# Kernel tuning notes

Measured on AMD Instinct MI355X. Metric: run time of the kernel, lower is better.

Reference implementation:

```python
import jax, jax.numpy as jnp
import numpy as np

N_PROBLEMS = 20000
N_SKILLS = 1000
EMB_SIZE = 128
TIME_LOG = 5.0
B, L = 64, 1024


def setup_inputs() -> dict:
    key = jax.random.key(0)
    ks = jax.random.split(key, 10)
    skills = jax.random.randint(ks[0], (B, L), 0, N_SKILLS)
    problems = jax.random.randint(ks[1], (B, L), 0, N_PROBLEMS)
    labels = jax.random.randint(ks[2], (B, L), 0, 2)
    times = jnp.sort(jax.random.randint(ks[3], (B, L), 0, 1_000_000), axis=-1)
    inp = jnp.stack([skills, problems, labels, times], axis=1)  # [B,4,L]
    std = 0.01
    return {
        "input": inp,
        "problem_base": std * jax.random.normal(ks[4], (N_PROBLEMS, 1), jnp.float32),
        "skill_base": std * jax.random.normal(ks[5], (N_SKILLS, 1), jnp.float32),
        "alpha_inter": std * jax.random.normal(ks[6], (N_SKILLS * 2, EMB_SIZE), jnp.float32),
        "alpha_skill": std * jax.random.normal(ks[7], (N_SKILLS, EMB_SIZE), jnp.float32),
        "beta_inter": std * jax.random.normal(ks[8], (N_SKILLS * 2, EMB_SIZE), jnp.float32),
        "beta_skill": std * jax.random.normal(ks[9], (N_SKILLS, EMB_SIZE), jnp.float32),
    }


def reference(input, problem_base, skill_base, alpha_inter, alpha_skill, beta_inter, beta_skill):
    skills = input[:, 0]    # [B,L]
    problems = input[:, 1]
    labels = input[:, 2]
    times = input[:, 3]

    mask_labels = labels * (labels < 2).astype(labels.dtype)
    inters = skills + mask_labels * N_SKILLS  # [B,L] in [0, 2*N_SKILLS)

    # pairwise Hawkes excitation / decay scores: [B,L,L]
    alphas = jnp.einsum('bie,bje->bij', alpha_inter[inters], alpha_skill[skills])
    betas = jnp.einsum('bie,bje->bij', beta_inter[inters], beta_skill[skills])
    betas = jnp.clip(betas + 1.0, 0.0, 10.0)

    dt = jnp.abs(times[:, :, None] - times[:, None, :]).astype(jnp.float32)
    log_dt = jnp.log(dt + 1e-10) / np.log(TIME_LOG)

    cross_effects = alphas * jnp.exp(-betas * log_dt)

    seq_len = skills.shape[1]
    # keep strictly-upper-triangular entries (source i before target j)
    keep = jnp.triu(jnp.ones((seq_len, seq_len), dtype=bool), k=1)
    sum_t = jnp.where(keep[None], cross_effects, 0.0).sum(axis=-2)  # [B,L]

    problem_bias = problem_base[problems][..., 0]
    skill_bias = skill_base[skills][..., 0]
    return jax.nn.sigmoid(problem_bias + skill_bias + sum_t)
```

## Files before the change

kernel.cpp:

```cpp
#include <hip/hip_runtime.h>
#include <hip/hip_bf16.h>

#define NB   64
#define SL   1024
#define EMB  128
#define NSK  1000
#define TI   64
#define SB   136
#define NS   2

#define AI_OFF 0
#define BI_OFF 256000
#define AS_OFF 512000
#define BS_OFF 640000
#define TB_ELEMS 768000
#define ACC_BYTE_OFF (TB_ELEMS * 2)

using short8  = __attribute__((ext_vector_type(8))) short;
using floatx4 = __attribute__((ext_vector_type(4))) float;

#define INV_LOG2_5 0.43067655807339306f

__device__ inline unsigned cvt2(float x, float y) {
    float2 f; f.x = x; f.y = y;
    __hip_bfloat162 h = __float22bfloat162_rn(f);
    unsigned u; __builtin_memcpy(&u, &h, sizeof(u));
    return u;
}

extern "C" __global__ __launch_bounds__(256)
void cvt_tables(const float* __restrict__ ai, const float* __restrict__ bi,
                const float* __restrict__ as, const float* __restrict__ bs,
                unsigned short* __restrict__ dst)
{
    const int t = blockIdx.x * 256 + threadIdx.x;
    const long e = (long)t * 8;
    const float* src;
    if      (e < 256000) src = ai + e;
    else if (e < 512000) src = bi + (e - 256000);
    else if (e < 640000) src = as + (e - 512000);
    else                 src = bs + (e - 640000);
    float4 f0 = *(const float4*)src;
    float4 f1 = *(const float4*)(src + 4);
    uint4 pk;
    pk.x = cvt2(f0.x, f0.y); pk.y = cvt2(f0.z, f0.w);
    pk.z = cvt2(f1.x, f1.y); pk.w = cvt2(f1.z, f1.w);
    *(uint4*)(dst + e) = pk;
}

__device__ float fixup_pair(const float* __restrict__ air,
                            const float* __restrict__ bir,
                            const float* __restrict__ asr,
                            const float* __restrict__ bsr) {
    float da = 0.f, db = 0.f;
    for (int k = 0; k < EMB; ++k) {
        da += air[k] * asr[k];
        db += bir[k] * bsr[k];
    }
    float beta = fminf(fmaxf(db + 1.f, 0.f), 10.f);
    return da * __expf(beta * 14.30676558073393f);
}

extern "C" __global__ __launch_bounds__(256, 4)
void hawkes_main(const int*   __restrict__ inp,
                 const unsigned short* __restrict__ tb,
                 float*       __restrict__ acc)
{
    __shared__ unsigned short lA[2][TI][SB];

    const int bid  = blockIdx.x;
    const int b    = bid & (NB - 1);
    const int r    = bid >> 6;
    const int jt   = 15 - (r >> 1);
    const int s    = r & 1;
    const int tid  = threadIdx.x;
    const int w    = tid >> 6;
    const int l    = tid & 63;
    const int quad = l >> 4;
    const int col  = l & 15;

    const int* __restrict__ binp = inp + b * 4 * SL;

    const int jlane = jt * TI + w * 16 + col;
    const int sk_j  = binp[jlane];
    const int tj    = binp[3 * SL + jlane];

    const unsigned short* asr16 = tb + AS_OFF + (long)sk_j * EMB + quad * 8;
    const unsigned short* bsr16 = tb + BS_OFF + (long)sk_j * EMB + quad * 8;
    short8 bfa[4], bfb[4];
#pragma unroll
    for (int ks = 0; ks < 4; ++ks) {
        bfa[ks] = *(const short8*)(asr16 + ks * 32);
        bfb[ks] = *(const short8*)(bsr16 + ks * 32);
    }

    const int srow = tid >> 2;
    const int sq   = tid & 3;
    unsigned short* dA = &lA[0][srow][sq * 32];
    unsigned short* dB = &lA[1][srow][sq * 32];

    float sum = 0.f;

    if (s <= jt) {
        uint4 pa0, pa1, pa2, pa3, pb0, pb1, pb2, pb3;
        {
            const int irow  = s * TI + srow;
            const int ski   = binp[irow];
            const int li    = binp[2 * SL + irow];
            const long intr = ski + (long)li * NSK;
            const unsigned short* sA  = tb + AI_OFF + intr * EMB + sq * 32;
            const unsigned short* sBm = tb + BI_OFF + intr * EMB + sq * 32;
            pa0 = *(const uint4*)(sA);      pa1 = *(const uint4*)(sA + 8);
            pa2 = *(const uint4*)(sA + 16); pa3 = *(const uint4*)(sA + 24);
            pb0 = *(const uint4*)(sBm);     pb1 = *(const uint4*)(sBm + 8);
            pb2 = *(const uint4*)(sBm + 16);pb3 = *(const uint4*)(sBm + 24);
        }

        for (int it = s; it <= jt; it += NS) {
            __syncthreads();
            *(uint4*)(dA)      = pa0; *(uint4*)(dA + 8)  = pa1;
            *(uint4*)(dA + 16) = pa2; *(uint4*)(dA + 24) = pa3;
            *(uint4*)(dB)      = pb0; *(uint4*)(dB + 8)  = pb1;
            *(uint4*)(dB + 16) = pb2; *(uint4*)(dB + 24) = pb3;

            if (it + NS <= jt) {
                const int irow  = (it + NS) * TI + srow;
                const int ski   = binp[irow];
                const int li    = binp[2 * SL + irow];
                const long intr = ski + (long)li * NSK;
                const unsigned short* sA  = tb + AI_OFF + intr * EMB + sq * 32;
                const unsigned short* sBm = tb + BI_OFF + intr * EMB + sq * 32;
                pa0 = *(const uint4*)(sA);      pa1 = *(const uint4*)(sA + 8);
                pa2 = *(const uint4*)(sA + 16); pa3 = *(const uint4*)(sA + 24);
                pb0 = *(const uint4*)(sBm);     pb1 = *(const uint4*)(sBm + 8);
                pb2 = *(const uint4*)(sBm + 16);pb3 = *(const uint4*)(sBm + 24);
            }
            __syncthreads();

            const int itb = it * TI;
#pragma unroll
            for (int isub = 0; isub < 4; ++isub) {
                floatx4 aa = {0.f, 0.f, 0.f, 0.f};
                floatx4 bb = {0.f, 0.f, 0.f, 0.f};
#pragma unroll
                for (int ks = 0; ks < 4; ++ks) {
                    const int k0 = ks * 32 + quad * 8;
                    short8 av = *(const short8*)&lA[0][isub * 16 + col][k0];
                    short8 bv = *(const short8*)&lA[1][isub * 16 + col][k0];
                    aa = __builtin_amdgcn_mfma_f32_16x16x32_bf16(av, bfa[ks], aa, 0, 0, 0);
                    bb = __builtin_amdgcn_mfma_f32_16x16x32_bf16(bv, bfb[ks], bb, 0, 0, 0);
                }
                const int ibase = itb + isub * 16 + quad * 4;
                const int4 t4 = *(const int4*)(binp + 3 * SL + ibase);
#pragma unroll
                for (int rr = 0; rr < 4; ++rr) {
                    const int ti = (rr == 0) ? t4.x : (rr == 1) ? t4.y : (rr == 2) ? t4.z : t4.w;
                    const int dt = tj - ti;
                    float lc  = __log2f((float)dt);
                    float nb  = fminf(fmaxf(bb[rr] + 1.f, 0.f), 10.f) * (-INV_LOG2_5);
                    float arg = (dt > 0) ? nb * lc : -__builtin_inff();
                    sum += aa[rr] * exp2f(arg);
                }
            }
        }
    }

    sum += __shfl_xor(sum, 16, 64);
    sum += __shfl_xor(sum, 32, 64);

    if (quad == 0) {
        acc[(((long)s * NB + b) << 10) + jlane] = sum;
    }
}

extern "C" __global__ __launch_bounds__(256)
void hawkes_finalize(const int* __restrict__ inp, const float* __restrict__ pbase,
                     const float* __restrict__ sbase,
                     const float* __restrict__ ai, const float* __restrict__ as,
                     const float* __restrict__ bi, const float* __restrict__ bs,
                     const float* __restrict__ acc, float* __restrict__ out)
{
    const int t = blockIdx.x * 256 + threadIdx.x;
    const int b = t >> 10, j = t & (SL - 1);
    const int* binp = inp + b * 4 * SL;
    const int tj   = binp[3 * SL + j];
    const int sk_j = binp[j];

    float corr = 0.f;
    for (int i = j - 1; i >= 0 && binp[3 * SL + i] == tj; --i) {
        const int ski = binp[i], li = binp[2 * SL + i];
        const long intr = ski + (long)li * NSK;
        corr += fixup_pair(ai + intr * EMB, bi + intr * EMB,
                           as + (long)sk_j * EMB, bs + (long)sk_j * EMB);
    }

    float sum = acc[t] + acc[NB * SL + t] + corr;
    const float x = pbase[binp[SL + j]] + sbase[sk_j] + sum;
    out[t] = 1.f / (1.f + __expf(-x));
}

extern "C" void kernel_launch(void* const* d_in, const int* in_sizes, int n_in,
                              void* d_out, int out_size, void* d_ws, size_t ws_size,
                              hipStream_t stream) {
    const int*   inp = (const int*)d_in[0];
    const float* pb  = (const float*)d_in[1];
    const float* sb  = (const float*)d_in[2];
    const float* ai  = (const float*)d_in[3];
    const float* as  = (const float*)d_in[4];
    const float* bi  = (const float*)d_in[5];
    const float* bs  = (const float*)d_in[6];

    unsigned short* tb  = (unsigned short*)d_ws;
    float*          acc = (float*)((char*)d_ws + ACC_BYTE_OFF);

    cvt_tables<<<dim3(96000 / 256), dim3(256), 0, stream>>>(ai, bi, as, bs, tb);
    hawkes_main<<<dim3(NB * 16 * NS), dim3(256), 0, stream>>>(inp, tb, acc);
    hawkes_finalize<<<dim3(NB * SL / 256), dim3(256), 0, stream>>>(
        inp, pb, sb, ai, as, bi, bs, acc, (float*)d_out);
}
```

Baseline: 114.8 us.

## Split tile staging into two half-tile phases with XOR-swizzled LDS and finer prefetch

Restructures the main loop so each 64-row tile is processed as two 32-row halves in separate LDS buffers. Writing one half and loading the next overlaps with the MFMA compute on the other half. The LDS layout drops padding in favour of an XOR swizzle to avoid bank conflicts, and each thread now loads one table row rather than two, which cuts register pressure. Smaller tweaks fold the +1 bias into the accumulator init, switch to the raw exp2 intrinsic, and vectorise the finalize fixup dot product. It adds an extra barrier per tile and more complex indexing.

```diff
diff --git a/kernel.cpp b/kernel.cpp
--- a/kernel.cpp
+++ b/kernel.cpp
@@ -6,7 +6,6 @@
 #define EMB  128
 #define NSK  1000
 #define TI   64
-#define SB   136
 #define NS   2
 
 #define AI_OFF 0
@@ -53,12 +52,76 @@
                             const float* __restrict__ asr,
                             const float* __restrict__ bsr) {
     float da = 0.f, db = 0.f;
-    for (int k = 0; k < EMB; ++k) {
-        da += air[k] * asr[k];
-        db += bir[k] * bsr[k];
+#pragma unroll 8
+    for (int k = 0; k < EMB; k += 4) {
+        float4 a  = *(const float4*)(air + k);
+        float4 s  = *(const float4*)(asr + k);
+        float4 bq = *(const float4*)(bir + k);
+        float4 tt = *(const float4*)(bsr + k);
+        da += a.x * s.x + a.y * s.y + a.z * s.z + a.w * s.w;
+        db += bq.x * tt.x + bq.y * tt.y + bq.z * tt.z + bq.w * tt.w;
     }
     float beta = fminf(fmaxf(db + 1.f, 0.f), 10.f);
     return da * __expf(beta * 14.30676558073393f);
+}
+
+struct Stage { uint4 a0, a1, a2, a3; };
+
+__device__ __forceinline__ Stage stage_load(const int* __restrict__ binp,
+                                            const unsigned short* __restrict__ tb,
+                                            int ib, int row, int m, int sq)
+{
+    const int irow  = ib + row;
+    const int ski   = binp[irow];
+    const int li    = binp[2 * SL + irow];
+    const long intr = ski + (long)li * NSK;
+    const unsigned short* src = tb + (m ? BI_OFF : AI_OFF) + intr * EMB + sq * 32;
+    Stage s;
+    s.a0 = *(const uint4*)(src);
+    s.a1 = *(const uint4*)(src + 8);
+    s.a2 = *(const uint4*)(src + 16);
+    s.a3 = *(const uint4*)(src + 24);
+    return s;
+}
+
+__device__ __forceinline__ void stage_write(char* buf, int wbase, const Stage& s) {
+    *(uint4*)(buf + wbase)              = s.a0;
+    *(uint4*)(buf + wbase + 128)        = s.a1;
+    *(uint4*)(buf + (wbase ^ 16))       = s.a2;
+    *(uint4*)(buf + (wbase ^ 16) + 128) = s.a3;
+}
+
+__device__ __forceinline__ float phase_compute(const char* __restrict__ buf,
+                                               const int* __restrict__ binp,
+                                               const short8 bfa[4], const short8 bfb[4],
+                                               const int roff[4],
+                                               int ib, int tj, int quad)
+{
+    float psum = 0.f;
+#pragma unroll
+    for (int isub = 0; isub < 2; ++isub) {
+        floatx4 aa = {0.f, 0.f, 0.f, 0.f};
+        floatx4 bb = {1.f, 1.f, 1.f, 1.f};
+#pragma unroll
+        for (int ks = 0; ks < 4; ++ks) {
+            short8 av = *(const short8*)(buf + isub * 4096 + roff[ks]);
+            short8 bv = *(const short8*)(buf + 8192 + isub * 4096 + roff[ks]);
+            aa = __builtin_amdgcn_mfma_f32_16x16x32_bf16(av, bfa[ks], aa, 0, 0, 0);
+            bb = __builtin_amdgcn_mfma_f32_16x16x32_bf16(bv, bfb[ks], bb, 0, 0, 0);
+        }
+        const int ibase = ib + isub * 16 + quad * 4;
+        const int4 t4 = *(const int4*)(binp + 3 * SL + ibase);
+#pragma unroll
+        for (int rr = 0; rr < 4; ++rr) {
+            const int ti = (rr == 0) ? t4.x : (rr == 1) ? t4.y : (rr == 2) ? t4.z : t4.w;
+            const int dt = tj - ti;
+            float lc  = __log2f((float)dt);
+            float nb  = fminf(fmaxf(bb[rr], 0.f), 10.f) * (-INV_LOG2_5);
+            float arg = (dt > 0) ? nb * lc : -__builtin_inff();
+            psum += aa[rr] * __builtin_amdgcn_exp2f(arg);
+        }
+    }
+    return psum;
 }
 
 extern "C" __global__ __launch_bounds__(256, 4)
@@ -66,7 +129,8 @@
                  const unsigned short* __restrict__ tb,
                  float*       __restrict__ acc)
 {
-    __shared__ unsigned short lA[2][TI][SB];
+    __shared__ uint4 lds4[2048];
+    char* ldsc = (char*)lds4;
 
     const int bid  = blockIdx.x;
     const int b    = bid & (NB - 1);
@@ -85,83 +149,58 @@
     const int sk_j  = binp[jlane];
     const int tj    = binp[3 * SL + jlane];
 
-    const unsigned short* asr16 = tb + AS_OFF + (long)sk_j * EMB + quad * 8;
-    const unsigned short* bsr16 = tb + BS_OFF + (long)sk_j * EMB + quad * 8;
     short8 bfa[4], bfb[4];
-#pragma unroll
-    for (int ks = 0; ks < 4; ++ks) {
-        bfa[ks] = *(const short8*)(asr16 + ks * 32);
-        bfb[ks] = *(const short8*)(bsr16 + ks * 32);
-    }
-
-    const int srow = tid >> 2;
-    const int sq   = tid & 3;
-    unsigned short* dA = &lA[0][srow][sq * 32];
-    unsigned short* dB = &lA[1][srow][sq * 32];
+    {
+        const unsigned short* asr16 = tb + AS_OFF + (long)sk_j * EMB + quad * 8;
+        const unsigned short* bsr16 = tb + BS_OFF + (long)sk_j * EMB + quad * 8;
+#pragma unroll
+        for (int ks = 0; ks < 4; ++ks) {
+            bfa[ks] = *(const short8*)(asr16 + ks * 32);
+            bfb[ks] = *(const short8*)(bsr16 + ks * 32);
+        }
+    }
+
+    int roff[4];
+    {
+        const int qh = quad >> 1, ql = quad & 1, c7 = col & 7;
+#pragma unroll
+        for (int ks = 0; ks < 4; ++ks)
+            roff[ks] = col * 256 + ql * 128 + (((2 * ks + qh) ^ c7) << 4);
+    }
+
+    const int ri    = tid >> 2;
+    const int m     = ri >> 5;
+    const int row   = ri & 31;
+    const int sq    = tid & 3;
+    const int wbase = m * 8192 + row * 256 + ((((2 * sq) ^ (row & 7))) << 4);
 
     float sum = 0.f;
 
     if (s <= jt) {
-        uint4 pa0, pa1, pa2, pa3, pb0, pb1, pb2, pb3;
-        {
-            const int irow  = s * TI + srow;
-            const int ski   = binp[irow];
-            const int li    = binp[2 * SL + irow];
-            const long intr = ski + (long)li * NSK;
-            const unsigned short* sA  = tb + AI_OFF + intr * EMB + sq * 32;
-            const unsigned short* sBm = tb + BI_OFF + intr * EMB + sq * 32;
-            pa0 = *(const uint4*)(sA);      pa1 = *(const uint4*)(sA + 8);
-            pa2 = *(const uint4*)(sA + 16); pa3 = *(const uint4*)(sA + 24);
-            pb0 = *(const uint4*)(sBm);     pb1 = *(const uint4*)(sBm + 8);
-            pb2 = *(const uint4*)(sBm + 16);pb3 = *(const uint4*)(sBm + 24);
-        }
-
-        for (int it = s; it <= jt; it += NS) {
+        const int ntiles = ((jt - s) >> 1) + 1;
+        int ib = s * TI;
+
+        Stage rA = stage_load(binp, tb, ib, row, m, sq);
+        stage_write(ldsc, wbase, rA);
+        Stage rB = stage_load(binp, tb, ib + 32, row, m, sq);
+
+        for (int t = 0; t < ntiles; ++t) {
+            const int ibn   = ib + NS * TI;
+            const bool more = (t + 1 < ntiles);
+
             __syncthreads();
-            *(uint4*)(dA)      = pa0; *(uint4*)(dA + 8)  = pa1;
-            *(uint4*)(dA + 16) = pa2; *(uint4*)(dA + 24) = pa3;
-            *(uint4*)(dB)      = pb0; *(uint4*)(dB + 8)  = pb1;
-            *(uint4*)(dB + 16) = pb2; *(uint4*)(dB + 24) = pb3;
-
-            if (it + NS <= jt) {
-                const int irow  = (it + NS) * TI + srow;
-                const int ski   = binp[irow];
-                const int li    = binp[2 * SL + irow];
-                const long intr = ski + (long)li * NSK;
-                const unsigned short* sA  = tb + AI_OFF + intr * EMB + sq * 32;
-                const unsigned short* sBm = tb + BI_OFF + intr * EMB + sq * 32;
-                pa0 = *(const uint4*)(sA);      pa1 = *(const uint4*)(sA + 8);
-                pa2 = *(const uint4*)(sA + 16); pa3 = *(const uint4*)(sA + 24);
-                pb0 = *(const uint4*)(sBm);     pb1 = *(const uint4*)(sBm + 8);
-                pb2 = *(const uint4*)(sBm + 16);pb3 = *(const uint4*)(sBm + 24);
+            stage_write(ldsc + 16384, wbase, rB);
+            if (more) rA = stage_load(binp, tb, ibn, row, m, sq);
+            sum += phase_compute(ldsc, binp, bfa, bfb, roff, ib, tj, quad);
+
+            __syncthreads();
+            if (more) {
+                stage_write(ldsc, wbase, rA);
+                rB = stage_load(binp, tb, ibn + 32, row, m, sq);
             }
-            __syncthreads();
-
-            const int itb = it * TI;
-#pragma unroll
-            for (int isub = 0; isub < 4; ++isub) {
-                floatx4 aa = {0.f, 0.f, 0.f, 0.f};
-                floatx4 bb = {0.f, 0.f, 0.f, 0.f};
-#pragma unroll
-                for (int ks = 0; ks < 4; ++ks) {
-                    const int k0 = ks * 32 + quad * 8;
-                    short8 av = *(const short8*)&lA[0][isub * 16 + col][k0];
-                    short8 bv = *(const short8*)&lA[1][isub * 16 + col][k0];
-                    aa = __builtin_amdgcn_mfma_f32_16x16x32_bf16(av, bfa[ks], aa, 0, 0, 0);
-                    bb = __builtin_amdgcn_mfma_f32_16x16x32_bf16(bv, bfb[ks], bb, 0, 0, 0);
-                }
-                const int ibase = itb + isub * 16 + quad * 4;
-                const int4 t4 = *(const int4*)(binp + 3 * SL + ibase);
-#pragma unroll
-                for (int rr = 0; rr < 4; ++rr) {
-                    const int ti = (rr == 0) ? t4.x : (rr == 1) ? t4.y : (rr == 2) ? t4.z : t4.w;
-                    const int dt = tj - ti;
-                    float lc  = __log2f((float)dt);
-                    float nb  = fminf(fmaxf(bb[rr] + 1.f, 0.f), 10.f) * (-INV_LOG2_5);
-                    float arg = (dt > 0) ? nb * lc : -__builtin_inff();
-                    sum += aa[rr] * exp2f(arg);
-                }
-            }
+            sum += phase_compute(ldsc + 16384, binp, bfa, bfb, roff, ib + 32, tj, quad);
+
+            ib = ibn;
         }
     }
 
```

Result: no change. 116.2 us (+1.2%).

## Keep target skill fragments in registers and stream source rows directly from global

Applied to the files above, without the earlier changes.

The main kernel now loads all 64 target skill rows for the tile once into swizzled LDS, then into registers (4 strips × 4 k-steps). Each wave takes its own 16 source rows per iteration straight from global memory, so the per-iteration LDS staging and the two barriers are gone. Each wave computes a 16×64 block using 4 strips of MFMAs, and the per-wave partial sums are combined through LDS at the end. The changes also fold the +1 into the bb accumulator init, use the raw exp2 builtin, vectorise the finalize fixup dot product, and lower the occupancy hint to 2. The cost is much higher register pressure and global loads that are no longer prefetched.

```diff
diff --git a/kernel.cpp b/kernel.cpp
--- a/kernel.cpp
+++ b/kernel.cpp
@@ -6,7 +6,6 @@
 #define EMB  128
 #define NSK  1000
 #define TI   64
-#define SB   136
 #define NS   2
 
 #define AI_OFF 0
@@ -15,6 +14,11 @@
 #define BS_OFF 640000
 #define TB_ELEMS 768000
 #define ACC_BYTE_OFF (TB_ELEMS * 2)
+
+#define AI_B 0
+#define BI_B 512000
+#define AS_B 1024000
+#define BS_B 1280000
 
 using short8  = __attribute__((ext_vector_type(8))) short;
 using floatx4 = __attribute__((ext_vector_type(4))) float;
@@ -53,20 +57,26 @@
                             const float* __restrict__ asr,
                             const float* __restrict__ bsr) {
     float da = 0.f, db = 0.f;
-    for (int k = 0; k < EMB; ++k) {
-        da += air[k] * asr[k];
-        db += bir[k] * bsr[k];
+#pragma unroll 8
+    for (int k = 0; k < EMB; k += 4) {
+        float4 a  = *(const float4*)(air + k);
+        float4 s  = *(const float4*)(asr + k);
+        float4 bq = *(const float4*)(bir + k);
+        float4 tt = *(const float4*)(bsr + k);
+        da += a.x * s.x + a.y * s.y + a.z * s.z + a.w * s.w;
+        db += bq.x * tt.x + bq.y * tt.y + bq.z * tt.z + bq.w * tt.w;
     }
     float beta = fminf(fmaxf(db + 1.f, 0.f), 10.f);
     return da * __expf(beta * 14.30676558073393f);
 }
 
-extern "C" __global__ __launch_bounds__(256, 4)
+extern "C" __global__ __launch_bounds__(256, 2)
 void hawkes_main(const int*   __restrict__ inp,
                  const unsigned short* __restrict__ tb,
                  float*       __restrict__ acc)
 {
-    __shared__ unsigned short lA[2][TI][SB];
+    __shared__ uint4 ldsq[2048];
+    char* ldsc = (char*)ldsq;
 
     const int bid  = blockIdx.x;
     const int b    = bid & (NB - 1);
@@ -78,98 +88,120 @@
     const int l    = tid & 63;
     const int quad = l >> 4;
     const int col  = l & 15;
+    const int wrow = w * 16;
 
     const int* __restrict__ binp = inp + b * 4 * SL;
-
-    const int jlane = jt * TI + w * 16 + col;
-    const int sk_j  = binp[jlane];
-    const int tj    = binp[3 * SL + jlane];
-
-    const unsigned short* asr16 = tb + AS_OFF + (long)sk_j * EMB + quad * 8;
-    const unsigned short* bsr16 = tb + BS_OFF + (long)sk_j * EMB + quad * 8;
-    short8 bfa[4], bfb[4];
-#pragma unroll
-    for (int ks = 0; ks < 4; ++ks) {
-        bfa[ks] = *(const short8*)(asr16 + ks * 32);
-        bfb[ks] = *(const short8*)(bsr16 + ks * 32);
-    }
-
-    const int srow = tid >> 2;
-    const int sq   = tid & 3;
-    unsigned short* dA = &lA[0][srow][sq * 32];
-    unsigned short* dB = &lA[1][srow][sq * 32];
-
-    float sum = 0.f;
-
-    if (s <= jt) {
-        uint4 pa0, pa1, pa2, pa3, pb0, pb1, pb2, pb3;
-        {
-            const int irow  = s * TI + srow;
-            const int ski   = binp[irow];
-            const int li    = binp[2 * SL + irow];
-            const long intr = ski + (long)li * NSK;
-            const unsigned short* sA  = tb + AI_OFF + intr * EMB + sq * 32;
-            const unsigned short* sBm = tb + BI_OFF + intr * EMB + sq * 32;
-            pa0 = *(const uint4*)(sA);      pa1 = *(const uint4*)(sA + 8);
-            pa2 = *(const uint4*)(sA + 16); pa3 = *(const uint4*)(sA + 24);
-            pb0 = *(const uint4*)(sBm);     pb1 = *(const uint4*)(sBm + 8);
-            pb2 = *(const uint4*)(sBm + 16);pb3 = *(const uint4*)(sBm + 24);
-        }
-
-        for (int it = s; it <= jt; it += NS) {
-            __syncthreads();
-            *(uint4*)(dA)      = pa0; *(uint4*)(dA + 8)  = pa1;
-            *(uint4*)(dA + 16) = pa2; *(uint4*)(dA + 24) = pa3;
-            *(uint4*)(dB)      = pb0; *(uint4*)(dB + 8)  = pb1;
-            *(uint4*)(dB + 16) = pb2; *(uint4*)(dB + 24) = pb3;
-
-            if (it + NS <= jt) {
-                const int irow  = (it + NS) * TI + srow;
-                const int ski   = binp[irow];
-                const int li    = binp[2 * SL + irow];
-                const long intr = ski + (long)li * NSK;
-                const unsigned short* sA  = tb + AI_OFF + intr * EMB + sq * 32;
-                const unsigned short* sBm = tb + BI_OFF + intr * EMB + sq * 32;
-                pa0 = *(const uint4*)(sA);      pa1 = *(const uint4*)(sA + 8);
-                pa2 = *(const uint4*)(sA + 16); pa3 = *(const uint4*)(sA + 24);
-                pb0 = *(const uint4*)(sBm);     pb1 = *(const uint4*)(sBm + 8);
-                pb2 = *(const uint4*)(sBm + 16);pb3 = *(const uint4*)(sBm + 24);
+    const char* __restrict__ tbc = (const char*)tb;
+
+    const int jbase = jt * TI;
+
+    int tjv[4];
+#pragma unroll
+    for (int strip = 0; strip < 4; ++strip)
+        tjv[strip] = binp[3 * SL + jbase + strip * 16 + col];
+
+    {
+        const int row  = tid >> 2;
+        const int sq   = tid & 3;
+        const int skj  = binp[jbase + row];
+        const char* srcA = tbc + AS_B + (long)skj * 256 + sq * 64;
+        const char* srcB = tbc + BS_B + (long)skj * 256 + sq * 64;
+        uint4 qa[4], qb[4];
+#pragma unroll
+        for (int u = 0; u < 4; ++u) {
+            qa[u] = *(const uint4*)(srcA + u * 16);
+            qb[u] = *(const uint4*)(srcB + u * 16);
+        }
+        const int rx = (row & 15) << 4;
+        const int wb = row * 256;
+#pragma unroll
+        for (int u = 0; u < 4; ++u) {
+            const int slot = (((4 * sq + u) << 4) ^ rx);
+            *(uint4*)(ldsc + wb + slot)         = qa[u];
+            *(uint4*)(ldsc + 16384 + wb + slot) = qb[u];
+        }
+    }
+    __syncthreads();
+
+    short8 bfa[4][4], bfb[4][4];
+#pragma unroll
+    for (int strip = 0; strip < 4; ++strip) {
+        const int row   = strip * 16 + col;
+        const int rbase = row * 256;
+        const int rx    = (row & 15) << 4;
+#pragma unroll
+        for (int ks = 0; ks < 4; ++ks) {
+            const int cb = ((quad + ks * 4) << 4) ^ rx;
+            bfa[strip][ks] = *(const short8*)(ldsc + rbase + cb);
+            bfb[strip][ks] = *(const short8*)(ldsc + 16384 + rbase + cb);
+        }
+    }
+
+    int intrv[8];
+#pragma unroll
+    for (int tt = 0; tt < 8; ++tt) {
+        const int arow = (s + 2 * tt) * TI + wrow + col;
+        intrv[tt] = binp[arow] + binp[2 * SL + arow] * NSK;
+    }
+
+    float sum[4] = {0.f, 0.f, 0.f, 0.f};
+
+#pragma unroll 1
+    for (int it = s; it <= jt; it += NS) {
+        const int tt = (it - s) >> 1;
+        const long ab = (long)intrv[tt] * 256 + quad * 16;
+        const char* pA = tbc + AI_B + ab;
+        const char* pB = tbc + BI_B + ab;
+        short8 av[4], bv[4];
+#pragma unroll
+        for (int ks = 0; ks < 4; ++ks) {
+            av[ks] = *(const short8*)(pA + ks * 64);
+            bv[ks] = *(const short8*)(pB + ks * 64);
+        }
+        const int4 t4 = *(const int4*)(binp + 3 * SL + it * TI + wrow + quad * 4);
+
+        floatx4 aa[4], bb[4];
+#pragma unroll
+        for (int strip = 0; strip < 4; ++strip) {
+            aa[strip] = floatx4{0.f, 0.f, 0.f, 0.f};
+            bb[strip] = floatx4{1.f, 1.f, 1.f, 1.f};
+        }
+#pragma unroll
+        for (int ks = 0; ks < 4; ++ks) {
+#pragma unroll
+            for (int strip = 0; strip < 4; ++strip) {
+                aa[strip] = __builtin_amdgcn_mfma_f32_16x16x32_bf16(av[ks], bfa[strip][ks], aa[strip], 0, 0, 0);
+                bb[strip] = __builtin_amdgcn_mfma_f32_16x16x32_bf16(bv[ks], bfb[strip][ks], bb[strip], 0, 0, 0);
             }
-            __syncthreads();
-
-            const int itb = it * TI;
-#pragma unroll
-            for (int isub = 0; isub < 4; ++isub) {
-                floatx4 aa = {0.f, 0.f, 0.f, 0.f};
-                floatx4 bb = {0.f, 0.f, 0.f, 0.f};
-#pragma unroll
-                for (int ks = 0; ks < 4; ++ks) {
-                    const int k0 = ks * 32 + quad * 8;
-                    short8 av = *(const short8*)&lA[0][isub * 16 + col][k0];
-                    short8 bv = *(const short8*)&lA[1][isub * 16 + col][k0];
-                    aa = __builtin_amdgcn_mfma_f32_16x16x32_bf16(av, bfa[ks], aa, 0, 0, 0);
-                    bb = __builtin_amdgcn_mfma_f32_16x16x32_bf16(bv, bfb[ks], bb, 0, 0, 0);
-                }
-                const int ibase = itb + isub * 16 + quad * 4;
-                const int4 t4 = *(const int4*)(binp + 3 * SL + ibase);
-#pragma unroll
-                for (int rr = 0; rr < 4; ++rr) {
-                    const int ti = (rr == 0) ? t4.x : (rr == 1) ? t4.y : (rr == 2) ? t4.z : t4.w;
-                    const int dt = tj - ti;
-                    float lc  = __log2f((float)dt);
-                    float nb  = fminf(fmaxf(bb[rr] + 1.f, 0.f), 10.f) * (-INV_LOG2_5);
-                    float arg = (dt > 0) ? nb * lc : -__builtin_inff();
-                    sum += aa[rr] * exp2f(arg);
-                }
+        }
+
+#pragma unroll
+        for (int strip = 0; strip < 4; ++strip) {
+            const int tjs = tjv[strip];
+#pragma unroll
+            for (int rr = 0; rr < 4; ++rr) {
+                const int ti = (rr == 0) ? t4.x : (rr == 1) ? t4.y : (rr == 2) ? t4.z : t4.w;
+                const int dt = tjs - ti;
+                float lc  = __log2f((float)dt);
+                float nb  = fminf(fmaxf(bb[strip][rr], 0.f), 10.f) * (-INV_LOG2_5);
+                float arg = (dt > 0) ? nb * lc : -__builtin_inff();
+                sum[strip] += aa[strip][rr] * __builtin_amdgcn_exp2f(arg);
             }
         }
     }
 
-    sum += __shfl_xor(sum, 16, 64);
-    sum += __shfl_xor(sum, 32, 64);
-
-    if (quad == 0) {
-        acc[(((long)s * NB + b) << 10) + jlane] = sum;
+#pragma unroll
+    for (int strip = 0; strip < 4; ++strip) {
+        sum[strip] += __shfl_xor(sum[strip], 16, 64);
+        sum[strip] += __shfl_xor(sum[strip], 32, 64);
+    }
+    __syncthreads();
+    float* red = (float*)ldsc;
+    red[w * 64 + quad * 16 + col] = sum[quad];
+    __syncthreads();
+    if (w == 0) {
+        const float tot = red[l] + red[64 + l] + red[128 + l] + red[192 + l];
+        acc[(((long)s * NB + b) << 10) + jbase + l] = tot;
     }
 }
 
```

Result: slower. 119.2 us (+3.8%).
